# Performance work log

Measured on AMD Instinct MI355X. Metric: run time of the kernel, lower is better.

The kernel has to match this reference:

```python
import jax, jax.numpy as jnp
import numpy as np

INPUT_SIZE, HIDDEN_SIZE, OUTPUT_SIZE = 64, 256, 1


def setup_inputs() -> dict:
    key = jax.random.key(0)
    ks = jax.random.split(key, 7)
    B, T, I, H, O = 256, 512, INPUT_SIZE, HIDDEN_SIZE, OUTPUT_SIZE
    s_ih = 1.0 / np.sqrt(H)
    return {
        "x": jax.random.normal(ks[0], (B, T, I), dtype=jnp.float32),
        # PyTorch GRUCell layout: rows ordered [reset, update, new], shape [3H, in]
        "w_ih": jax.random.uniform(ks[1], (3 * H, I), jnp.float32, -s_ih, s_ih),
        "w_hh": jax.random.uniform(ks[2], (3 * H, H), jnp.float32, -s_ih, s_ih),
        "b_ih": jax.random.uniform(ks[3], (3 * H,), jnp.float32, -s_ih, s_ih),
        "b_hh": jax.random.uniform(ks[4], (3 * H,), jnp.float32, -s_ih, s_ih),
        "w_out": jax.random.uniform(ks[5], (O, H), jnp.float32, -s_ih, s_ih),
        "b_out": jax.random.uniform(ks[6], (O,), jnp.float32, -s_ih, s_ih),
    }


def reference(x, w_ih, w_hh, b_ih, b_hh, w_out, b_out):
    B, T, I = x.shape
    H = w_hh.shape[1]
    # Precompute all input-side gate projections in one big GEMM: [T, B, 3H]
    gi_all = jnp.einsum("bti,gi->tbg", x, w_ih) + b_ih

    def step(h, gi):
        gh = h @ w_hh.T + b_hh  # [B, 3H]
        i_r, i_z, i_n = jnp.split(gi, 3, axis=-1)
        h_r, h_z, h_n = jnp.split(gh, 3, axis=-1)
        r = jax.nn.sigmoid(i_r + h_r)
        z = jax.nn.sigmoid(i_z + h_z)
        n = jnp.tanh(i_n + r * h_n)
        h_new = (1.0 - z) * n + z * h
        return h_new, h_new

    h0 = jnp.zeros((B, H), dtype=x.dtype)
    _, hs = jax.lax.scan(step, h0, gi_all)  # hs: [T, B, H]
    outs = jnp.einsum("tbh,oh->tbo", hs, w_out) + b_out  # [T, B, O]
    return outs
```

## Files before the change

### kernel.cpp

```cpp
#include <hip/hip_runtime.h>

typedef _Float16 half8 __attribute__((ext_vector_type(8)));
typedef _Float16 f16x2 __attribute__((ext_vector_type(2)));
typedef _Float16 f16x4 __attribute__((ext_vector_type(4)));
typedef float floatx4 __attribute__((ext_vector_type(4)));

#define NB 256
#define NT 512
#define NI 64
#define NH 256
#define NSEQ 16
#define QB 4
#define NGRP (NB / NSEQ)
#define NBLK (NGRP * QB)
#define THR 256
#define HS 344

#define WB_N (480 * 512)
#define HD_N ((size_t)NT * NB * NH)
#define HX_N ((size_t)2 * NB * NH)

__global__ __launch_bounds__(256) void gru_prep_kernel(
    const float* __restrict__ w_ih, const float* __restrict__ w_hh,
    _Float16* __restrict__ wb, int* __restrict__ flags)
{
  if (blockIdx.x == 0 && threadIdx.x < NBLK) flags[threadIdx.x * 32] = 0;
  int n = blockIdx.x * 256 + threadIdx.x;
  if (n >= WB_N) return;
  int i = n & 7, l = (n >> 3) & 63, f = n >> 9;
  int q = l >> 4, col = l & 15;
  int tt, kb, gate;
  if (f < 160)      { tt = f / 10;               kb = f % 10;        gate = 0; }
  else if (f < 320) { int f2 = f - 160; tt = f2 / 10; kb = f2 % 10;  gate = 1; }
  else if (f < 448) { int f3 = f - 320; tt = f3 / 8;  kb = f3 % 8;   gate = 2; }
  else              { int f4 = f - 448; tt = f4 / 2;  kb = 8 + (f4 & 1); gate = 3; }
  int j = (tt & 15) * 16 + col;
  int k = kb * 32 + q * 8 + i;
  float v;
  if (gate == 0)      v = (k < 256) ? w_hh[(0   + j) * 256 + k] : w_ih[(0   + j) * 64 + (k - 256)];
  else if (gate == 1) v = (k < 256) ? w_hh[(256 + j) * 256 + k] : w_ih[(256 + j) * 64 + (k - 256)];
  else if (gate == 2) v = w_hh[(512 + j) * 256 + k];
  else                v = w_ih[(512 + j) * 64 + (k - 256)];
  wb[n] = (_Float16)v;
}

__device__ __forceinline__ float sigm(float v) {
  return __builtin_amdgcn_rcpf(1.0f + __expf(-v));
}
__device__ __forceinline__ float tanh_f(float v) {
  return 1.0f - 2.0f * __builtin_amdgcn_rcpf(1.0f + __expf(2.0f * v));
}

#define MFMA16(a, b, c) __builtin_amdgcn_mfma_f32_16x16x32_f16(a, b, c, 0, 0, 0)
#define FDOT(W, X, A) __builtin_amdgcn_fdot2(__builtin_bit_cast(f16x2, W), \
                                             __builtin_bit_cast(f16x2, X), A, false)

typedef unsigned long long u64;
__device__ __forceinline__ void hx_store8(u64* p, u64 v) {
  __hip_atomic_store(p, v, __ATOMIC_RELAXED, __HIP_MEMORY_SCOPE_AGENT);
}
__device__ __forceinline__ u64 hx_load8(const u64* p) {
  return __hip_atomic_load(p, __ATOMIC_RELAXED, __HIP_MEMORY_SCOPE_AGENT);
}

__global__ __launch_bounds__(THR) void gru_kernel(
    const float* __restrict__ x,
    const float* __restrict__ b_ih,
    const float* __restrict__ b_hh,
    const _Float16* __restrict__ wb,
    _Float16* __restrict__ HD,
    _Float16* __restrict__ HX,
    int* __restrict__ flags)
{
  __shared__ __align__(16) _Float16 H[2][NSEQ][HS];
  __shared__ __align__(16) _Float16 WB[120 * 512];

  const int tid  = threadIdx.x;
  const int lane = tid & 63;
  const int w    = tid >> 6;
  const int q    = lane >> 4;
  const int col  = lane & 15;
  const int gidx = blockIdx.x & 15;
  const int qb   = blockIdx.x >> 4;
  const int b0   = gidx * NSEQ;
  const int tt   = qb * 4 + w;
  const int j    = tt * 16 + col;

  {
    const float4* src4 = (const float4*)wb;
    float4* dst4 = (float4*)WB;
    #pragma unroll
    for (int it = 0; it < 30; ++it) {
      int d = tid + it * THR;
      int slot = d >> 6, elem = d & 63;
      int tau = slot / 30, r = slot % 30;
      int gt = qb * 4 + tau;
      int f = (r < 10) ? (gt * 10 + r)
            : (r < 20) ? (160 + gt * 10 + (r - 10))
            : (r < 28) ? (320 + gt * 8 + (r - 20))
                       : (448 + gt * 2 + (r - 28));
      dst4[d] = src4[(size_t)f * 64 + elem];
    }
  }
  const _Float16* wB = WB + (size_t)(w * 30) * 512 + (size_t)lane * 8;

  const float br   = b_ih[j] + b_hh[j];
  const float bz   = b_ih[256 + j] + b_hh[256 + j];
  const float bin_ = b_ih[512 + j];
  const float bhn  = b_hh[512 + j];

  {
    float4* hz = (float4*)H;
    #pragma unroll
    for (int it = 0; it < 6; ++it) {
      int idx = tid + it * THR;
      if (idx < (int)(sizeof(H) / 16)) hz[idx] = float4{0, 0, 0, 0};
    }
  }
  const int r16 = tid >> 4, c4 = (tid & 15) * 4;
  const float* xbase = x + (size_t)(b0 + r16) * (NT * NI) + c4;
  __syncthreads();
  {
    float4 v = *(const float4*)xbase;
    f16x4 xh; xh[0] = (_Float16)v.x; xh[1] = (_Float16)v.y;
    xh[2] = (_Float16)v.z; xh[3] = (_Float16)v.w;
    *(f16x4*)&H[0][r16][256 + c4] = xh;
  }
  float h0 = 0.0f, h1 = 0.0f, h2 = 0.0f, h3 = 0.0f;
  __syncthreads();

  for (int t = 0; t < NT; ++t) {
    const int cur = t & 1, nxt = cur ^ 1;

    const _Float16* hrow = &H[cur][col][q * 8];
    floatx4 cR = {0,0,0,0}, cZ = {0,0,0,0}, cN = {0,0,0,0}, cI = {0,0,0,0};
    #pragma unroll
    for (int k = 0; k < 8; ++k) {
      half8 a = *(const half8*)(hrow + k * 32);
      cR = MFMA16(a, *(const half8*)(wB + (size_t)(k)      * 512), cR);
      cZ = MFMA16(a, *(const half8*)(wB + (size_t)(10 + k) * 512), cZ);
      cN = MFMA16(a, *(const half8*)(wB + (size_t)(20 + k) * 512), cN);
    }
    { half8 a = *(const half8*)(hrow + 8 * 32);
      cR = MFMA16(a, *(const half8*)(wB + (size_t)8  * 512), cR);
      cZ = MFMA16(a, *(const half8*)(wB + (size_t)18 * 512), cZ);
      cI = MFMA16(a, *(const half8*)(wB + (size_t)28 * 512), cI); }
    { half8 a = *(const half8*)(hrow + 9 * 32);
      cR = MFMA16(a, *(const half8*)(wB + (size_t)9  * 512), cR);
      cZ = MFMA16(a, *(const half8*)(wB + (size_t)19 * 512), cZ);
      cI = MFMA16(a, *(const half8*)(wB + (size_t)29 * 512), cI); }

#define GATE(m, hvar) { \
    float rr = sigm(cR[m] + br); \
    float zz = sigm(cZ[m] + bz); \
    float nn = tanh_f(cI[m] + bin_ + rr * (cN[m] + bhn)); \
    hvar = (1.0f - zz) * nn + zz * hvar; \
    H[nxt][q * 4 + (m)][j] = (_Float16)hvar; }
    GATE(0, h0) GATE(1, h1) GATE(2, h2) GATE(3, h3)
#undef GATE
    __syncthreads();

    if (t + 1 < NT) {
      {
        u64 v = *(const u64*)&H[nxt][r16][qb * 64 + (tid & 15) * 4];
        hx_store8((u64*)(HX + ((size_t)cur * NB + b0 + r16) * NH + qb * 64 + (tid & 15) * 4), v);
      }
      asm volatile("s_waitcnt vmcnt(0)" ::: "memory");
      __syncthreads();
      if (tid == 0) atomicAdd(&flags[(gidx * QB + qb) * 32], 1);

      float4 xv = *(const float4*)(xbase + (size_t)(t + 1) * NI);
      if (t > 0 && tid < 128) {
        int row = tid >> 3, c8 = tid & 7;
        float4 hv = *(const float4*)&H[cur][row][qb * 64 + c8 * 8];
        *(float4*)(HD + ((size_t)(t - 1) * NB + b0 + row) * NH + qb * 64 + c8 * 8) = hv;
      }

      if (tid < QB && tid != qb) {
        while (atomicAdd(&flags[(gidx * QB + tid) * 32], 0) < t + 1)
          __builtin_amdgcn_s_sleep(2);
      }
      __syncthreads();

      {
        const u64* hxb = (const u64*)(HX + (size_t)cur * NB * NH);
        int pq0i = 0, pq1i = 1, pq2i = 2;
        int pq0 = pq0i + (pq0i >= qb ? 1 : 0);
        int pq1 = pq1i + (pq1i >= qb ? 1 : 0);
        int pq2 = pq2i + (pq2i >= qb ? 1 : 0);
        int row = tid >> 4, ca = tid & 15;
        size_t rb = (size_t)(b0 + row) * (NH / 4);
        u64 v0 = hx_load8(hxb + rb + pq0 * 16 + ca);
        u64 v1 = hx_load8(hxb + rb + pq1 * 16 + ca);
        u64 v2 = hx_load8(hxb + rb + pq2 * 16 + ca);
        *(u64*)&H[nxt][row][pq0 * 64 + ca * 4] = v0;
        *(u64*)&H[nxt][row][pq1 * 64 + ca * 4] = v1;
        *(u64*)&H[nxt][row][pq2 * 64 + ca * 4] = v2;
      }
      {
        f16x4 xh; xh[0] = (_Float16)xv.x; xh[1] = (_Float16)xv.y;
        xh[2] = (_Float16)xv.z; xh[3] = (_Float16)xv.w;
        *(f16x4*)&H[nxt][r16][256 + c4] = xh;
      }
      __syncthreads();
    } else {
      if (tid < 128) {
        int row = tid >> 3, c8 = tid & 7;
        float4 hv = *(const float4*)&H[cur][row][qb * 64 + c8 * 8];
        *(float4*)(HD + ((size_t)(t - 1) * NB + b0 + row) * NH + qb * 64 + c8 * 8) = hv;
      }
    }
  }

  if (tid < 128) {
    int row = tid >> 3, c8 = tid & 7;
    float4 hv = *(const float4*)&H[0][row][qb * 64 + c8 * 8];
    *(float4*)(HD + ((size_t)(NT - 1) * NB + b0 + row) * NH + qb * 64 + c8 * 8) = hv;
  }
}

__global__ __launch_bounds__(256) void gru_out_kernel(
    const _Float16* __restrict__ HD, const float* __restrict__ w_out,
    const float* __restrict__ b_out, float* __restrict__ out)
{
  __shared__ __align__(16) _Float16 WL[NH];
  int tid = threadIdx.x;
  WL[tid] = (_Float16)w_out[tid];
  __syncthreads();
  int gid = blockIdx.x * 256 + tid;
  const float4* hp = (const float4*)(HD + (size_t)gid * NH);
  const float4* wp = (const float4*)WL;
  float acc = 0.0f;
  #pragma unroll
  for (int i = 0; i < NH / 8; ++i) {
    float4 hv = hp[i];
    float4 wv = wp[i];
    acc = FDOT(hv.x, wv.x, acc);
    acc = FDOT(hv.y, wv.y, acc);
    acc = FDOT(hv.z, wv.z, acc);
    acc = FDOT(hv.w, wv.w, acc);
  }
  out[gid] = acc + b_out[0];
}

extern "C" void kernel_launch(void* const* d_in, const int* in_sizes, int n_in,
                              void* d_out, int out_size, void* d_ws, size_t ws_size,
                              hipStream_t stream) {
  const float* x     = (const float*)d_in[0];
  const float* w_ih  = (const float*)d_in[1];
  const float* w_hh  = (const float*)d_in[2];
  const float* b_ih  = (const float*)d_in[3];
  const float* b_hh  = (const float*)d_in[4];
  const float* w_out = (const float*)d_in[5];
  const float* b_out = (const float*)d_in[6];
  float* out = (float*)d_out;

  _Float16* wb = (_Float16*)d_ws;
  _Float16* HD = wb + WB_N;
  _Float16* HX = HD + HD_N;
  int* flags   = (int*)(HX + HX_N);

  gru_prep_kernel<<<(WB_N + 255) / 256, 256, 0, stream>>>(w_ih, w_hh, wb, flags);
  gru_kernel<<<NBLK, THR, 0, stream>>>(x, b_ih, b_hh, wb, HD, HX, flags);
  gru_out_kernel<<<(NT * NB) / 256, 256, 0, stream>>>(HD, w_out, b_out, out);
}
```

Baseline: 1.188 ms.

## Publish hidden-state slices directly from gate lanes and specialize waves for exchange

Each gate lane now writes its fp16 hidden value straight to the global exchange buffer. This removes one block barrier and the LDS-to-global copy before the flag is signaled. The flag update changes from an atomicAdd to a relaxed atomic store of the step count. Wave 0 handles the next-step x load and the HD writeback, while waves 1-3 each spin on one peer block's flag (without sleep) and copy only that peer's slice. This spreads the polling and makes the waits partly overlap, at the risk of many small 2-byte global stores and weaker memory-ordering guarantees.

```diff
diff --git a/kernel.cpp b/kernel.cpp
--- a/kernel.cpp
+++ b/kernel.cpp
@@ -56,11 +56,11 @@
                                              __builtin_bit_cast(f16x2, X), A, false)
 
 typedef unsigned long long u64;
-__device__ __forceinline__ void hx_store8(u64* p, u64 v) {
-  __hip_atomic_store(p, v, __ATOMIC_RELAXED, __HIP_MEMORY_SCOPE_AGENT);
-}
 __device__ __forceinline__ u64 hx_load8(const u64* p) {
   return __hip_atomic_load(p, __ATOMIC_RELAXED, __HIP_MEMORY_SCOPE_AGENT);
+}
+__device__ __forceinline__ void hx_store2(unsigned short* p, unsigned short v) {
+  __hip_atomic_store(p, v, __ATOMIC_RELAXED, __HIP_MEMORY_SCOPE_AGENT);
 }
 
 __global__ __launch_bounds__(THR) void gru_kernel(
@@ -118,10 +118,9 @@
     }
   }
   const int r16 = tid >> 4, c4 = (tid & 15) * 4;
-  const float* xbase = x + (size_t)(b0 + r16) * (NT * NI) + c4;
   __syncthreads();
   {
-    float4 v = *(const float4*)xbase;
+    float4 v = *(const float4*)(x + (size_t)(b0 + r16) * (NT * NI) + c4);
     f16x4 xh; xh[0] = (_Float16)v.x; xh[1] = (_Float16)v.y;
     xh[2] = (_Float16)v.z; xh[3] = (_Float16)v.w;
     *(f16x4*)&H[0][r16][256 + c4] = xh;
@@ -150,57 +149,62 @@
       cZ = MFMA16(a, *(const half8*)(wB + (size_t)19 * 512), cZ);
       cI = MFMA16(a, *(const half8*)(wB + (size_t)29 * 512), cI); }
 
+    const bool exch = (t + 1 < NT);
+
 #define GATE(m, hvar) { \
     float rr = sigm(cR[m] + br); \
     float zz = sigm(cZ[m] + bz); \
     float nn = tanh_f(cI[m] + bin_ + rr * (cN[m] + bhn)); \
     hvar = (1.0f - zz) * nn + zz * hvar; \
-    H[nxt][q * 4 + (m)][j] = (_Float16)hvar; }
+    _Float16 hf = (_Float16)hvar; \
+    H[nxt][q * 4 + (m)][j] = hf; \
+    if (exch) hx_store2((unsigned short*)(HX + ((size_t)cur * NB + b0 + q * 4 + (m)) * NH + j), \
+                        __builtin_bit_cast(unsigned short, hf)); }
     GATE(0, h0) GATE(1, h1) GATE(2, h2) GATE(3, h3)
 #undef GATE
-    __syncthreads();
-
-    if (t + 1 < NT) {
-      {
-        u64 v = *(const u64*)&H[nxt][r16][qb * 64 + (tid & 15) * 4];
-        hx_store8((u64*)(HX + ((size_t)cur * NB + b0 + r16) * NH + qb * 64 + (tid & 15) * 4), v);
-      }
+
+    if (exch) {
       asm volatile("s_waitcnt vmcnt(0)" ::: "memory");
       __syncthreads();
-      if (tid == 0) atomicAdd(&flags[(gidx * QB + qb) * 32], 1);
-
-      float4 xv = *(const float4*)(xbase + (size_t)(t + 1) * NI);
-      if (t > 0 && tid < 128) {
-        int row = tid >> 3, c8 = tid & 7;
-        float4 hv = *(const float4*)&H[cur][row][qb * 64 + c8 * 8];
-        *(float4*)(HD + ((size_t)(t - 1) * NB + b0 + row) * NH + qb * 64 + c8 * 8) = hv;
-      }
-
-      if (tid < QB && tid != qb) {
-        while (atomicAdd(&flags[(gidx * QB + tid) * 32], 0) < t + 1)
-          __builtin_amdgcn_s_sleep(2);
-      }
-      __syncthreads();
-
-      {
+      if (tid == 0)
+        __hip_atomic_store(&flags[(gidx * QB + qb) * 32], t + 1,
+                           __ATOMIC_RELAXED, __HIP_MEMORY_SCOPE_AGENT);
+
+      if (w == 0) {
+        float4 xq0, xq1, xq2, xq3;
+#define XL(e, dst) { int el = lane + (e) * 64; int row = el >> 4, c4i = (el & 15) * 4; \
+        dst = *(const float4*)(x + (size_t)(b0 + row) * (NT * NI) + (size_t)(t + 1) * NI + c4i); }
+        XL(0, xq0) XL(1, xq1) XL(2, xq2) XL(3, xq3)
+#undef XL
+        if (t > 0) {
+          #pragma unroll
+          for (int e = 0; e < 2; ++e) {
+            int el = lane + e * 64;
+            int row = el >> 3, c8 = el & 7;
+            float4 hv = *(const float4*)&H[cur][row][qb * 64 + c8 * 8];
+            *(float4*)(HD + ((size_t)(t - 1) * NB + b0 + row) * NH + qb * 64 + c8 * 8) = hv;
+          }
+        }
+#define XW(e, src) { int el = lane + (e) * 64; int row = el >> 4, c4i = (el & 15) * 4; \
+        f16x4 xh; xh[0] = (_Float16)src.x; xh[1] = (_Float16)src.y; \
+        xh[2] = (_Float16)src.z; xh[3] = (_Float16)src.w; \
+        *(f16x4*)&H[nxt][row][256 + c4i] = xh; }
+        XW(0, xq0) XW(1, xq1) XW(2, xq2) XW(3, xq3)
+#undef XW
+      } else {
+        const int pw = (qb + w) & 3;
+        const int* fp = &flags[(gidx * QB + pw) * 32];
+        while (__hip_atomic_load(fp, __ATOMIC_RELAXED, __HIP_MEMORY_SCOPE_AGENT) < t + 1) {}
         const u64* hxb = (const u64*)(HX + (size_t)cur * NB * NH);
-        int pq0i = 0, pq1i = 1, pq2i = 2;
-        int pq0 = pq0i + (pq0i >= qb ? 1 : 0);
-        int pq1 = pq1i + (pq1i >= qb ? 1 : 0);
-        int pq2 = pq2i + (pq2i >= qb ? 1 : 0);
-        int row = tid >> 4, ca = tid & 15;
-        size_t rb = (size_t)(b0 + row) * (NH / 4);
-        u64 v0 = hx_load8(hxb + rb + pq0 * 16 + ca);
-        u64 v1 = hx_load8(hxb + rb + pq1 * 16 + ca);
-        u64 v2 = hx_load8(hxb + rb + pq2 * 16 + ca);
-        *(u64*)&H[nxt][row][pq0 * 64 + ca * 4] = v0;
-        *(u64*)&H[nxt][row][pq1 * 64 + ca * 4] = v1;
-        *(u64*)&H[nxt][row][pq2 * 64 + ca * 4] = v2;
-      }
-      {
-        f16x4 xh; xh[0] = (_Float16)xv.x; xh[1] = (_Float16)xv.y;
-        xh[2] = (_Float16)xv.z; xh[3] = (_Float16)xv.w;
-        *(f16x4*)&H[nxt][r16][256 + c4] = xh;
+        int u0 = lane, u1 = lane + 64, u2 = lane + 128, u3 = lane + 192;
+        u64 v0 = hx_load8(hxb + (size_t)(b0 + (u0 >> 4)) * (NH / 4) + pw * 16 + (u0 & 15));
+        u64 v1 = hx_load8(hxb + (size_t)(b0 + (u1 >> 4)) * (NH / 4) + pw * 16 + (u1 & 15));
+        u64 v2 = hx_load8(hxb + (size_t)(b0 + (u2 >> 4)) * (NH / 4) + pw * 16 + (u2 & 15));
+        u64 v3 = hx_load8(hxb + (size_t)(b0 + (u3 >> 4)) * (NH / 4) + pw * 16 + (u3 & 15));
+        *(u64*)&H[nxt][u0 >> 4][pw * 64 + (u0 & 15) * 4] = v0;
+        *(u64*)&H[nxt][u1 >> 4][pw * 64 + (u1 & 15) * 4] = v1;
+        *(u64*)&H[nxt][u2 >> 4][pw * 64 + (u2 & 15) * 4] = v2;
+        *(u64*)&H[nxt][u3 >> 4][pw * 64 + (u3 & 15) * 4] = v3;
       }
       __syncthreads();
     } else {
@@ -209,6 +213,7 @@
         float4 hv = *(const float4*)&H[cur][row][qb * 64 + c8 * 8];
         *(float4*)(HD + ((size_t)(t - 1) * NB + b0 + row) * NH + qb * 64 + c8 * 8) = hv;
       }
+      __syncthreads();
     }
   }
 
```

After: 1.319 ms. +11.0%, slower.
